# Performance work log

Hardware: AMD Instinct MI355X
Metric: run time of the kernel (lower is better)

The kernel has to match this reference:

```python
import jax, jax.numpy as jnp
import numpy as np

X = 512; Y = 512; C = 3; NK = 15
DT = 0.2; DD = 2; SIGMA = 0.95
THETA_X = 2.0; N_EXP = 2.0
K_SIZE = 16

# mesh-grid positions, cell centers at +0.5 (matches construct_mesh_grid)
POS = (jnp.stack(jnp.meshgrid(jnp.arange(X), jnp.arange(Y), indexing='ij'), axis=-1) + 0.5).astype(jnp.float32)  # [X,Y,2]


def _dwconv(img, k):
    # img [X,Y,C'] -> depthwise 3x3 cross-correlation with 'same' zero padding (matches torch conv2d)
    z = img.transpose(2, 0, 1)[None]                      # [1,C',X,Y]
    kern = jnp.tile(k[None, None], (z.shape[1], 1, 1, 1))  # [C',1,3,3]
    out = jax.lax.conv_general_dilated(z, kern, (1, 1), 'SAME', feature_group_count=z.shape[1])
    return out[0].transpose(1, 2, 0)


def _sobel(img):
    # returns [X,Y,2,C'] with (sy, sx) stacked on axis 2, matching torch code order
    kx = jnp.array([[-1., 0., 1.], [-2., 0., 2.], [-1., 0., 1.]], jnp.float32)
    return jnp.stack([_dwconv(img, kx.T), _dwconv(img, kx)], axis=2)


def _reintegrate(grid, F):
    # Flow-Lenia reintegration tracking: 25 static roll offsets, fused accumulation
    ma = DD - SIGMA
    mu = POS[..., None] + jnp.clip(DT * F, -ma, ma)  # [X,Y,2,C]
    mu = jnp.clip(mu, SIGMA, X - SIGMA)
    clip_hi = min(1.0, 2.0 * SIGMA)
    inv_area = 1.0 / (4.0 * SIGMA ** 2)
    acc = jnp.zeros_like(grid)
    for dx in range(-DD, DD + 1):
        for dy in range(-DD, DD + 1):
            gridR = jnp.roll(grid, (dx, dy), (0, 1))
            muR = jnp.roll(mu, (dx, dy), (0, 1))
            sz = 0.5 - jnp.abs(POS[..., None] - muR) + SIGMA
            area = jnp.prod(jnp.clip(sz, 0.0, clip_hi), axis=2) * inv_area  # [X,Y,C]
            acc = acc + gridR * area
    return acc


def _forward(x, Ks, m, s, h, w_c1, c0):
    # spectral kernels: normalize, fftshift, fft2 (matches construct_kernels)
    Ksn = Ks / Ks.sum(axis=(0, 1), keepdims=True)
    fk = jnp.fft.fft2(jnp.fft.fftshift(Ksn, axes=(0, 1)), axes=(0, 1))  # [X,Y,NK] complex
    fXs = jnp.fft.fft2(x, axes=(0, 1))
    Us = jnp.fft.ifft2(fk * fXs[:, :, c0], axes=(0, 1)).real            # [X,Y,NK]
    # growth * h (note: h appears again inside w_c1, faithful to original double multiply)
    Gs = (jnp.exp(-(((Us - m) / s) ** 2) * 0.5) * 2.0 - 1.0) * h
    Hs = jnp.einsum('xyk,kc->xyc', Gs, w_c1)                             # [X,Y,C]
    grad_u = _sobel(Hs)                                                  # [X,Y,2,C]
    grad_x = _sobel(x.sum(-1, keepdims=True))                            # [X,Y,2,1]
    alpha = jnp.clip((x[:, :, None, :] / THETA_X) ** N_EXP, 0.0, 1.0)    # [X,Y,1,C]
    F = grad_u * (1.0 - alpha) - grad_x * alpha                          # [X,Y,2,C]
    return _reintegrate(x, F)


def setup_inputs() -> dict:
    key = jax.random.key(0)
    k1, k2, k3, k4, k5 = jax.random.split(key, 5)
    x = jax.random.uniform(k1, (X, Y, C), jnp.float32)
    # ring kernels per construct_kernels (non-sparse branch)
    mg = np.mgrid[-X // 2:X // 2, -Y // 2:Y // 2]
    base = np.linalg.norm(mg, axis=0).astype(np.float32)
    ks_list = []
    for i in range(NK):
        r = 0.6 + 0.04 * i
        D = base / ((K_SIZE + 15) * r)
        sig = 0.5 * (np.tanh(-(D - 1.0) * 10.0 / 2.0) + 1.0)
        bell = np.exp(-(D - 0.5) ** 2 / 0.15)
        ks_list.append(sig * bell)
    Ks = jnp.asarray(np.stack(ks_list, -1).astype(np.float32))
    m = 0.1 + 0.3 * jax.random.uniform(k2, (NK,), jnp.float32)
    s = 0.03 + 0.15 * jax.random.uniform(k3, (NK,), jnp.float32)
    h = 0.3 + 0.7 * jax.random.uniform(k4, (NK,), jnp.float32)
    c0 = jax.random.randint(k5, (NK,), 0, C, jnp.int32)
    c1 = jnp.arange(NK) % C
    w_c1 = jax.nn.one_hot(c1, C, dtype=jnp.float32) * h[:, None]
    return {"x": x, "Ks": Ks, "m": m, "s": s, "h": h, "w_c1": w_c1, "c0": c0}


def reference(x, Ks, m, s, h, w_c1, c0):
    return _forward(x, Ks, m, s, h, w_c1, c0)
```

## Files before the change

### kernel.cpp

```cpp
#include <hip/hip_runtime.h>
#include <math.h>

#define NPIX 262144
#define NKER 15
#define PI_F 3.14159265358979323846f
#define HW 264
#define NCOL 264
#define CS 578
#define SK(n) ((n) + ((n) >> 3))

__device__ __forceinline__ float2 cadd(float2 a, float2 b) { return make_float2(a.x + b.x, a.y + b.y); }
__device__ __forceinline__ float2 csub(float2 a, float2 b) { return make_float2(a.x - b.x, a.y - b.y); }
__device__ __forceinline__ float2 cmul(float2 a, float2 b) {
  return make_float2(a.x * b.x - a.y * b.y, a.x * b.y + a.y * b.x);
}

__device__ __forceinline__ void fft_roots(int lane, float2* w1, float2* wh) {
  float s, c;
  sincosf(-2.0f * PI_F * (float)lane / 512.0f, &s, &c);
  *w1 = make_float2(c, s);
  int h = lane & ~7;
  *wh = make_float2(__shfl(c, h, 64), __shfl(s, h, 64));
}

template <bool INV>
__device__ __forceinline__ void dft8(float2 a[8]) {
  const float R = 0.70710678118654752f;
  float2 t0 = cadd(a[0], a[4]), u0 = csub(a[0], a[4]);
  float2 t1 = cadd(a[1], a[5]), u1 = csub(a[1], a[5]);
  float2 t2 = cadd(a[2], a[6]), u2 = csub(a[2], a[6]);
  float2 t3 = cadd(a[3], a[7]), u3 = csub(a[3], a[7]);
  u1 = INV ? make_float2(R * (u1.x - u1.y), R * (u1.x + u1.y))
           : make_float2(R * (u1.x + u1.y), R * (u1.y - u1.x));
  u2 = INV ? make_float2(-u2.y, u2.x) : make_float2(u2.y, -u2.x);
  u3 = INV ? make_float2(-R * (u3.x + u3.y), R * (u3.x - u3.y))
           : make_float2(R * (u3.y - u3.x), -R * (u3.x + u3.y));
  float2 e0 = cadd(t0, t2), f0 = csub(t0, t2);
  float2 e1 = cadd(t1, t3), f1 = csub(t1, t3);
  f1 = INV ? make_float2(-f1.y, f1.x) : make_float2(f1.y, -f1.x);
  float2 g0 = cadd(u0, u2), h0 = csub(u0, u2);
  float2 g1 = cadd(u1, u3), h1 = csub(u1, u3);
  h1 = INV ? make_float2(-h1.y, h1.x) : make_float2(h1.y, -h1.x);
  a[0] = cadd(e0, e1); a[4] = csub(e0, e1);
  a[2] = cadd(f0, f1); a[6] = csub(f0, f1);
  a[1] = cadd(g0, g1); a[5] = csub(g0, g1);
  a[3] = cadd(h0, h1); a[7] = csub(h0, h1);
}

template <bool INV>
__device__ __forceinline__ void fft512_r8(float2 a[8], float2* buf, int lane,
                                          float2 w1, float2 wh) {
  float2 wa = INV ? make_float2(w1.x, -w1.y) : w1;
  float2 wb = INV ? make_float2(wh.x, -wh.y) : wh;
  dft8<INV>(a);
  {
    float2 tq = wa;
    a[1] = cmul(a[1], tq);
#pragma unroll
    for (int q = 2; q < 8; ++q) { tq = cmul(tq, wa); a[q] = cmul(a[q], tq); }
  }
#pragma unroll
  for (int q = 0; q < 8; ++q) buf[9 * lane + q] = a[q];
#pragma unroll
  for (int q = 0; q < 8; ++q) a[q] = buf[SK(lane + 64 * q)];
  dft8<INV>(a);
  {
    float2 tq = wb;
    a[1] = cmul(a[1], tq);
#pragma unroll
    for (int q = 2; q < 8; ++q) { tq = cmul(tq, wb); a[q] = cmul(a[q], tq); }
  }
  int h = lane & ~7;
  int b2 = 9 * h + (lane - h);
#pragma unroll
  for (int q = 0; q < 8; ++q) buf[b2 + 9 * q] = a[q];
#pragma unroll
  for (int q = 0; q < 8; ++q) a[q] = buf[SK(lane + 64 * q)];
  dft8<INV>(a);
}

__device__ __forceinline__ void split_store_halfplane(float2 a[8], float2* buf, int lane,
                                                      float2* d0, float2* d1) {
#pragma unroll
  for (int q = 0; q < 8; ++q) buf[SK(lane + 64 * q)] = a[q];
#pragma unroll
  for (int q = 0; q < 4; ++q) {
    int v = lane + 64 * q;
    int mir = (512 - v) & 511;
    float2 P = a[q];
    float2 Qc = buf[SK(mir)];
    float2 Q = make_float2(Qc.x, -Qc.y);
    d0[v] = make_float2(0.5f * (P.x + Q.x), 0.5f * (P.y + Q.y));
    d1[v] = make_float2(0.5f * (P.y - Q.y), -0.5f * (P.x - Q.x));
  }
  if (lane == 0) {
    float2 P = a[4];
    d0[256] = make_float2(P.x, 0.f);
    d1[256] = make_float2(P.y, 0.f);
  }
}

__global__ void rows_all(const float* __restrict__ Ks, const float* __restrict__ x,
                         float* __restrict__ partial, float2* __restrict__ AkH,
                         float2* __restrict__ AxH) {
  __shared__ float krow[512 * NKER];
  __shared__ float2 scr[4][CS];
  __shared__ float psum[480];
  int t = threadIdx.x, wave = t >> 6, lane = t & 63;
  float2 w1, wh;
  fft_roots(lane, &w1, &wh);
  if (blockIdx.x < 512) {
    int b = blockIdx.x;
    int rs = (b + 256) & 511;
    const float2* src = (const float2*)Ks + (size_t)rs * 3840;
    float2* kr2 = (float2*)krow;
#pragma unroll
    for (int i = 0; i < 15; ++i) kr2[t + 256 * i] = src[t + 256 * i];
    __syncthreads();
    for (int i = t; i < 480; i += 256) {
      int k = i >> 5, yg = i & 31;
      float s = 0.f;
      int base = yg * 16;
#pragma unroll
      for (int y = 0; y < 16; ++y) s += krow[(base + y) * NKER + k];
      psum[i] = s;
    }
#pragma unroll
    for (int si = 0; si < 2; ++si) {
      int slot = wave + 4 * si;
      int k1 = 2 * slot, k2 = k1 + 1;
      float2 a[8];
#pragma unroll
      for (int q = 0; q < 8; ++q) {
        int ys = (lane + 64 * q + 256) & 511;
        float re = krow[ys * NKER + k1];
        float im = (k2 < NKER) ? krow[ys * NKER + k2] : 0.f;
        a[q] = make_float2(re, im);
      }
      fft512_r8<false>(a, &scr[wave][0], lane, w1, wh);
      float2* d0 = AkH + ((size_t)k1 * 512 + b) * HW;
      float2* d1 = AkH + ((size_t)k2 * 512 + b) * HW;
      split_store_halfplane(a, &scr[wave][0], lane, d0, d1);
    }
    __syncthreads();
    if (t < NKER) {
      float s = 0.f;
#pragma unroll
      for (int g = 0; g < 32; ++g) s += psum[(t << 5) + g];
      partial[b * 16 + t] = s;
    }
  } else {
    int b = blockIdx.x - 512;
    int c = b >> 6;
    int rp = (b & 63) * 4 + wave;
    int r0 = rp, r1 = rp + 256;
    float2 a[8];
#pragma unroll
    for (int q = 0; q < 8; ++q) {
      int y = lane + 64 * q;
      a[q] = make_float2(x[((size_t)r0 * 512 + y) * 3 + c],
                         x[((size_t)r1 * 512 + y) * 3 + c]);
    }
    fft512_r8<false>(a, &scr[wave][0], lane, w1, wh);
    float2* d0 = AxH + ((size_t)c * 512 + r0) * HW;
    float2* d1 = AxH + ((size_t)c * 512 + r1) * HW;
    split_store_halfplane(a, &scr[wave][0], lane, d0, d1);
  }
}

__global__ void mid_cols(const float2* __restrict__ AxH, float2* __restrict__ XHt,
                         const float* __restrict__ partial, float* __restrict__ sums) {
  __shared__ float2 buf[8 * CS];
  __shared__ float red[512];
  int t = threadIdx.x;
  if (blockIdx.x == 99) {
    int k = t & 15, g = t >> 4;
    float acc = 0.f;
    for (int b = g; b < 512; b += 32) acc += partial[b * 16 + k];
    red[t] = acc;
    __syncthreads();
    if (t < 16) {
      float s = 0.f;
#pragma unroll
      for (int g2 = 0; g2 < 32; ++g2) s += red[g2 * 16 + t];
      sums[t] = s;
    }
    return;
  }
  int ch = blockIdx.x / 33, slab = blockIdx.x % 33;
  int col0 = slab * 8;
  int c = t >> 6, lane = t & 63;
  float2 w1, wh;
  fft_roots(lane, &w1, &wh);
  const float2* bx = AxH + (size_t)ch * 512 * HW;
#pragma unroll
  for (int u = 0; u < 8; ++u) {
    int idx = (u << 9) + t;
    int row = idx >> 3, cc = idx & 7;
    buf[cc * CS + SK(row)] = bx[(size_t)row * HW + col0 + cc];
  }
  __syncthreads();
  float2 a[8];
#pragma unroll
  for (int q = 0; q < 8; ++q) a[q] = buf[c * CS + SK(lane + 64 * q)];
  fft512_r8<false>(a, &buf[c * CS], lane, w1, wh);
  float2* dst = XHt + ((size_t)ch * NCOL + col0 + c) * 512;
#pragma unroll
  for (int q = 0; q < 8; ++q) dst[lane + 64 * q] = a[q];
}

__global__ void fused_cols(float2* __restrict__ AkH, const float2* __restrict__ XHt,
                           const int* __restrict__ c0) {
  __shared__ float2 buf[8 * CS];
  int t = threadIdx.x, col0 = blockIdx.x * 8, k = blockIdx.y;
  int c = t >> 6, lane = t & 63;
  float2 w1, wh;
  fft_roots(lane, &w1, &wh);
  float2* bk = AkH + (size_t)k * 512 * HW;
  const float2* xcol = XHt + ((size_t)c0[k] * NCOL + col0 + c) * 512;
  float2 xh[8];
#pragma unroll
  for (int q = 0; q < 8; ++q) xh[q] = xcol[lane + 64 * q];
#pragma unroll
  for (int u = 0; u < 8; ++u) {
    int idx = (u << 9) + t;
    int row = idx >> 3, cc = idx & 7;
    buf[cc * CS + SK(row)] = bk[(size_t)row * HW + col0 + cc];
  }
  __syncthreads();
  float2 a[8];
#pragma unroll
  for (int q = 0; q < 8; ++q) a[q] = buf[c * CS + SK(lane + 64 * q)];
  fft512_r8<false>(a, &buf[c * CS], lane, w1, wh);
#pragma unroll
  for (int q = 0; q < 8; ++q) a[q] = cmul(a[q], xh[q]);
  fft512_r8<true>(a, &buf[c * CS], lane, w1, wh);
#pragma unroll
  for (int q = 0; q < 8; ++q) buf[c * CS + SK(lane + 64 * q)] = a[q];
  __syncthreads();
#pragma unroll
  for (int u = 0; u < 8; ++u) {
    int idx = (u << 9) + t;
    int row = idx >> 3, cc = idx & 7;
    bk[(size_t)row * HW + col0 + cc] = buf[cc * CS + SK(row)];
  }
}

__global__ void irows_growth_combine(const float2* __restrict__ AkH,
                                     const float* __restrict__ sums,
                                     const float* __restrict__ m, const float* __restrict__ s,
                                     const float* __restrict__ h, const float* __restrict__ w,
                                     float* __restrict__ Hs) {
  __shared__ float2 scr[4][CS];
  __shared__ float accL[4][3][512];
  __shared__ float mk[16], isk[16], hk[16], wk[16][3], sck[16];
  int t = threadIdx.x, wave = t >> 6, lane = t & 63;
  int row = blockIdx.x;
  if (t < NKER) {
    mk[t] = m[t]; isk[t] = 1.0f / s[t]; hk[t] = h[t];
    sck[t] = 1.0f / (sums[t] * 262144.0f);
    wk[t][0] = w[t * 3 + 0]; wk[t][1] = w[t * 3 + 1]; wk[t][2] = w[t * 3 + 2];
  }
  __syncthreads();
  float2 w1, wh;
  fft_roots(lane, &w1, &wh);
  float acc[3][8];
#pragma unroll
  for (int cc = 0; cc < 3; ++cc)
#pragma unroll
    for (int q = 0; q < 8; ++q) acc[cc][q] = 0.f;
  for (int si = 0; si < 2; ++si) {
    int slot = wave + 4 * si;
    int k1 = 2 * slot, k2 = 2 * slot + 1;
    bool dual = (k2 < NKER);
    const float2* p1 = AkH + ((size_t)k1 * 512 + row) * HW;
    const float2* p2 = AkH + ((size_t)(dual ? k2 : k1) * 512 + row) * HW;
    float2 a[8];
#pragma unroll
    for (int q = 0; q < 8; ++q) {
      int v = lane + 64 * q;
      if (v <= 256) {
        float2 A1 = p1[v];
        float2 A2 = dual ? p2[v] : make_float2(0.f, 0.f);
        a[q] = make_float2(A1.x - A2.y, A1.y + A2.x);
      } else {
        int mi = 512 - v;
        float2 A1 = p1[mi];
        float2 A2 = dual ? p2[mi] : make_float2(0.f, 0.f);
        a[q] = make_float2(A1.x + A2.y, -A1.y + A2.x);
      }
    }
    fft512_r8<true>(a, &scr[wave][0], lane, w1, wh);
    float m1 = mk[k1], i1 = isk[k1], h1 = hk[k1], s1 = sck[k1];
    float w10 = wk[k1][0], w11 = wk[k1][1], w12 = wk[k1][2];
#pragma unroll
    for (int q = 0; q < 8; ++q) {
      float tt = (a[q].x * s1 - m1) * i1;
      float g = (expf(-0.5f * tt * tt) * 2.0f - 1.0f) * h1;
      acc[0][q] += g * w10; acc[1][q] += g * w11; acc[2][q] += g * w12;
    }
    if (dual) {
      float m2 = mk[k2], i2 = isk[k2], h2 = hk[k2], s2 = sck[k2];
      float w20 = wk[k2][0], w21 = wk[k2][1], w22 = wk[k2][2];
#pragma unroll
      for (int q = 0; q < 8; ++q) {
        float tt = (a[q].y * s2 - m2) * i2;
        float g = (expf(-0.5f * tt * tt) * 2.0f - 1.0f) * h2;
        acc[0][q] += g * w20; acc[1][q] += g * w21; acc[2][q] += g * w22;
      }
    }
  }
#pragma unroll
  for (int cc = 0; cc < 3; ++cc)
#pragma unroll
    for (int q = 0; q < 8; ++q) accL[wave][cc][lane + 64 * q] = acc[cc][q];
  __syncthreads();
#pragma unroll
  for (int cc = 0; cc < 3; ++cc) {
#pragma unroll
    for (int rep = 0; rep < 2; ++rep) {
      int p = t + (rep << 8);
      float v = accL[0][cc][p] + accL[1][cc][p] + accL[2][cc][p] + accL[3][cc][p];
      Hs[(size_t)cc * NPIX + (size_t)row * 512 + p] = v;
    }
  }
}

__global__ void flow_reint(const float* __restrict__ x, const float* __restrict__ Hs,
                           float* __restrict__ out) {
  __shared__ float muT[20 * 20 * 6];
  __shared__ float xT[20 * 20 * 3];
  int ox = (blockIdx.x >> 5) << 4;
  int oy = (blockIdx.x & 31) << 4;
  for (int i = threadIdx.x; i < 400; i += 256) {
    int hi = i / 20, hj = i % 20;
    int qx = (ox - 2 + hi) & 511, qy = (oy - 2 + hj) & 511;
    float syH0 = 0.f, syH1 = 0.f, syH2 = 0.f;
    float sxH0 = 0.f, sxH1 = 0.f, sxH2 = 0.f;
    float syX = 0.f, sxX = 0.f;
#pragma unroll
    for (int di = -1; di <= 1; ++di) {
#pragma unroll
      for (int dj = -1; dj <= 1; ++dj) {
        if (di == 0 && dj == 0) continue;
        int xi = qx + di, yj = qy + dj;
        if ((unsigned)xi >= 512u || (unsigned)yj >= 512u) continue;
        float wy = (float)di * ((dj == 0) ? 2.f : 1.f);
        float wx = (float)dj * ((di == 0) ? 2.f : 1.f);
        int q = (xi << 9) | yj;
        float h0 = Hs[q], h1 = Hs[NPIX + q], h2 = Hs[2 * NPIX + q];
        syH0 += wy * h0; syH1 += wy * h1; syH2 += wy * h2;
        sxH0 += wx * h0; sxH1 += wx * h1; sxH2 += wx * h2;
        float xs = x[(size_t)q * 3 + 0] + x[(size_t)q * 3 + 1] + x[(size_t)q * 3 + 2];
        syX += wy * xs; sxX += wx * xs;
      }
    }
    int qp = (qx << 9) | qy;
    float cxq = (float)qx + 0.5f, cyq = (float)qy + 0.5f;
    float syH[3] = {syH0, syH1, syH2};
    float sxH[3] = {sxH0, sxH1, sxH2};
    int b6 = i * 6, b3 = i * 3;
#pragma unroll
    for (int c = 0; c < 3; ++c) {
      float xc = x[(size_t)qp * 3 + c];
      xT[b3 + c] = xc;
      float tt = xc * 0.5f;
      float alpha = fminf(tt * tt, 1.0f);
      float F0 = syH[c] * (1.f - alpha) - syX * alpha;
      float F1 = sxH[c] * (1.f - alpha) - sxX * alpha;
      float m0 = cxq + fminf(fmaxf(0.2f * F0, -1.05f), 1.05f);
      float m1 = cyq + fminf(fmaxf(0.2f * F1, -1.05f), 1.05f);
      muT[b6 + c]     = fminf(fmaxf(m0, 0.95f), 511.05f);
      muT[b6 + 3 + c] = fminf(fmaxf(m1, 0.95f), 511.05f);
    }
  }
  __syncthreads();
  int o = threadIdx.x;
  int lx = o >> 4, ly = o & 15;
  int px_ = ox + lx, py_ = oy + ly;
  float cx = (float)px_ + 0.5f, cy = (float)py_ + 0.5f;
  float a0 = 0.f, a1 = 0.f, a2 = 0.f;
#pragma unroll
  for (int dx = -2; dx <= 2; ++dx) {
    int hi = lx + 2 - dx;
#pragma unroll
    for (int dy = -2; dy <= 2; ++dy) {
      int hj = ly + 2 - dy;
      int b6 = (hi * 20 + hj) * 6, b3 = (hi * 20 + hj) * 3;
      float wv;
      wv = fminf(fmaxf(1.45f - fabsf(cx - muT[b6 + 0]), 0.f), 1.f) *
           fminf(fmaxf(1.45f - fabsf(cy - muT[b6 + 3]), 0.f), 1.f);
      a0 += xT[b3 + 0] * wv;
      wv = fminf(fmaxf(1.45f - fabsf(cx - muT[b6 + 1]), 0.f), 1.f) *
           fminf(fmaxf(1.45f - fabsf(cy - muT[b6 + 4]), 0.f), 1.f);
      a1 += xT[b3 + 1] * wv;
      wv = fminf(fmaxf(1.45f - fabsf(cx - muT[b6 + 2]), 0.f), 1.f) *
           fminf(fmaxf(1.45f - fabsf(cy - muT[b6 + 5]), 0.f), 1.f);
      a2 += xT[b3 + 2] * wv;
    }
  }
  const float inv_area = 0.27700831f;
  size_t p = (size_t)((px_ << 9) | py_);
  out[p * 3 + 0] = a0 * inv_area;
  out[p * 3 + 1] = a1 * inv_area;
  out[p * 3 + 2] = a2 * inv_area;
}

extern "C" void kernel_launch(void* const* d_in, const int* in_sizes, int n_in,
                              void* d_out, int out_size, void* d_ws, size_t ws_size,
                              hipStream_t stream) {
  const float* x    = (const float*)d_in[0];
  const float* Ks   = (const float*)d_in[1];
  const float* m    = (const float*)d_in[2];
  const float* s    = (const float*)d_in[3];
  const float* h    = (const float*)d_in[4];
  const float* w_c1 = (const float*)d_in[5];
  const int*   c0   = (const int*)d_in[6];
  float* out = (float*)d_out;

  char* ws = (char*)d_ws;
  size_t off = 0;
  float* sums    = (float*)(ws + off); off += 1024;
  float* partial = (float*)(ws + off); off += 512 * 16 * 4;
  float2* AxH  = (float2*)(ws + off); off += (size_t)3 * 512 * HW * 8;
  float2* XHt  = (float2*)(ws + off); off += (size_t)3 * NCOL * 512 * 8;
  float2* AkH  = (float2*)(ws + off); off += (size_t)16 * 512 * HW * 8;
  float*  Hs   = (float*)(ws + off);  off += (size_t)3 * NPIX * 4;

  rows_all<<<704, 256, 0, stream>>>(Ks, x, partial, AkH, AxH);
  mid_cols<<<100, 512, 0, stream>>>(AxH, XHt, partial, sums);
  fused_cols<<<dim3(33, NKER), 512, 0, stream>>>(AkH, XHt, c0);
  irows_growth_combine<<<512, 256, 0, stream>>>(AkH, sums, m, s, h, w_c1, Hs);
  flow_reint<<<1024, 256, 0, stream>>>(x, Hs, out);
}
```

Before: 135.4 us.

## Fuse x column FFT into per-kernel column pass and widen row blocks to 512 threads

Removes the separate mid_cols kernel and the XHt intermediate buffer. Each fused_cols block now redoes the column FFT of the matching x channel itself, and the kernel-sum reduction moves into an extra block column. rows_all and irows_growth_combine go to 512 threads so each wave handles one kernel pair instead of looping over two. This saves a launch and a global round trip, at the cost of 15x redundant x column FFTs and higher shared-memory and register use per block.

```diff
diff --git a/kernel.cpp b/kernel.cpp
--- a/kernel.cpp
+++ b/kernel.cpp
@@ -5,7 +5,6 @@
 #define NKER 15
 #define PI_F 3.14159265358979323846f
 #define HW 264
-#define NCOL 264
 #define CS 578
 #define SK(n) ((n) + ((n) >> 3))
 
@@ -104,7 +103,7 @@
                          float* __restrict__ partial, float2* __restrict__ AkH,
                          float2* __restrict__ AxH) {
   __shared__ float krow[512 * NKER];
-  __shared__ float2 scr[4][CS];
+  __shared__ float2 scr[8][CS];
   __shared__ float psum[480];
   int t = threadIdx.x, wave = t >> 6, lane = t & 63;
   float2 w1, wh;
@@ -114,21 +113,18 @@
     int rs = (b + 256) & 511;
     const float2* src = (const float2*)Ks + (size_t)rs * 3840;
     float2* kr2 = (float2*)krow;
-#pragma unroll
-    for (int i = 0; i < 15; ++i) kr2[t + 256 * i] = src[t + 256 * i];
+    for (int i = t; i < 3840; i += 512) kr2[i] = src[i];
     __syncthreads();
-    for (int i = t; i < 480; i += 256) {
-      int k = i >> 5, yg = i & 31;
+    if (t < 480) {
+      int k = t >> 5, yg = t & 31;
       float s = 0.f;
       int base = yg * 16;
 #pragma unroll
       for (int y = 0; y < 16; ++y) s += krow[(base + y) * NKER + k];
-      psum[i] = s;
-    }
-#pragma unroll
-    for (int si = 0; si < 2; ++si) {
-      int slot = wave + 4 * si;
-      int k1 = 2 * slot, k2 = k1 + 1;
+      psum[t] = s;
+    }
+    {
+      int k1 = 2 * wave, k2 = k1 + 1;
       float2 a[8];
 #pragma unroll
       for (int q = 0; q < 8; ++q) {
@@ -150,9 +146,9 @@
       partial[b * 16 + t] = s;
     }
   } else {
-    int b = blockIdx.x - 512;
-    int c = b >> 6;
-    int rp = (b & 63) * 4 + wave;
+    int job = (blockIdx.x - 512) * 8 + wave;
+    int c = job >> 8;
+    int rp = job & 255;
     int r0 = rp, r1 = rp + 256;
     float2 a[8];
 #pragma unroll
@@ -168,12 +164,14 @@
   }
 }
 
-__global__ void mid_cols(const float2* __restrict__ AxH, float2* __restrict__ XHt,
-                         const float* __restrict__ partial, float* __restrict__ sums) {
+__global__ void fused_cols(float2* __restrict__ AkH, const float2* __restrict__ AxH,
+                           const int* __restrict__ c0, const float* __restrict__ partial,
+                           float* __restrict__ sums) {
   __shared__ float2 buf[8 * CS];
   __shared__ float red[512];
   int t = threadIdx.x;
-  if (blockIdx.x == 99) {
+  if (blockIdx.x == 33) {
+    if (blockIdx.y != 0) return;
     int k = t & 15, g = t >> 4;
     float acc = 0.f;
     for (int b = g; b < 512; b += 32) acc += partial[b * 16 + k];
@@ -187,12 +185,12 @@
     }
     return;
   }
-  int ch = blockIdx.x / 33, slab = blockIdx.x % 33;
-  int col0 = slab * 8;
+  int col0 = blockIdx.x * 8, k = blockIdx.y;
   int c = t >> 6, lane = t & 63;
   float2 w1, wh;
   fft_roots(lane, &w1, &wh);
-  const float2* bx = AxH + (size_t)ch * 512 * HW;
+  const float2* bx = AxH + (size_t)c0[k] * 512 * HW;
+  float2* bk = AkH + (size_t)k * 512 * HW;
 #pragma unroll
   for (int u = 0; u < 8; ++u) {
     int idx = (u << 9) + t;
@@ -200,27 +198,11 @@
     buf[cc * CS + SK(row)] = bx[(size_t)row * HW + col0 + cc];
   }
   __syncthreads();
-  float2 a[8];
-#pragma unroll
-  for (int q = 0; q < 8; ++q) a[q] = buf[c * CS + SK(lane + 64 * q)];
-  fft512_r8<false>(a, &buf[c * CS], lane, w1, wh);
-  float2* dst = XHt + ((size_t)ch * NCOL + col0 + c) * 512;
-#pragma unroll
-  for (int q = 0; q < 8; ++q) dst[lane + 64 * q] = a[q];
-}
-
-__global__ void fused_cols(float2* __restrict__ AkH, const float2* __restrict__ XHt,
-                           const int* __restrict__ c0) {
-  __shared__ float2 buf[8 * CS];
-  int t = threadIdx.x, col0 = blockIdx.x * 8, k = blockIdx.y;
-  int c = t >> 6, lane = t & 63;
-  float2 w1, wh;
-  fft_roots(lane, &w1, &wh);
-  float2* bk = AkH + (size_t)k * 512 * HW;
-  const float2* xcol = XHt + ((size_t)c0[k] * NCOL + col0 + c) * 512;
   float2 xh[8];
 #pragma unroll
-  for (int q = 0; q < 8; ++q) xh[q] = xcol[lane + 64 * q];
+  for (int q = 0; q < 8; ++q) xh[q] = buf[c * CS + SK(lane + 64 * q)];
+  fft512_r8<false>(xh, &buf[c * CS], lane, w1, wh);
+  __syncthreads();
 #pragma unroll
   for (int u = 0; u < 8; ++u) {
     int idx = (u << 9) + t;
@@ -251,7 +233,7 @@
                                      const float* __restrict__ m, const float* __restrict__ s,
                                      const float* __restrict__ h, const float* __restrict__ w,
                                      float* __restrict__ Hs) {
-  __shared__ float2 scr[4][CS];
+  __shared__ float2 scr[8][CS];
   __shared__ float accL[4][3][512];
   __shared__ float mk[16], isk[16], hk[16], wk[16][3], sck[16];
   int t = threadIdx.x, wave = t >> 6, lane = t & 63;
@@ -269,8 +251,8 @@
   for (int cc = 0; cc < 3; ++cc)
 #pragma unroll
     for (int q = 0; q < 8; ++q) acc[cc][q] = 0.f;
-  for (int si = 0; si < 2; ++si) {
-    int slot = wave + 4 * si;
+  {
+    int slot = wave;
     int k1 = 2 * slot, k2 = 2 * slot + 1;
     bool dual = (k2 < NKER);
     const float2* p1 = AkH + ((size_t)k1 * 512 + row) * HW;
@@ -310,19 +292,24 @@
       }
     }
   }
-#pragma unroll
-  for (int cc = 0; cc < 3; ++cc)
-#pragma unroll
-    for (int q = 0; q < 8; ++q) accL[wave][cc][lane + 64 * q] = acc[cc][q];
+  if (wave < 4) {
+#pragma unroll
+    for (int cc = 0; cc < 3; ++cc)
+#pragma unroll
+      for (int q = 0; q < 8; ++q) accL[wave][cc][lane + 64 * q] = acc[cc][q];
+  }
+  __syncthreads();
+  if (wave >= 4) {
+#pragma unroll
+    for (int cc = 0; cc < 3; ++cc)
+#pragma unroll
+      for (int q = 0; q < 8; ++q) accL[wave - 4][cc][lane + 64 * q] += acc[cc][q];
+  }
   __syncthreads();
 #pragma unroll
   for (int cc = 0; cc < 3; ++cc) {
-#pragma unroll
-    for (int rep = 0; rep < 2; ++rep) {
-      int p = t + (rep << 8);
-      float v = accL[0][cc][p] + accL[1][cc][p] + accL[2][cc][p] + accL[3][cc][p];
-      Hs[(size_t)cc * NPIX + (size_t)row * 512 + p] = v;
-    }
+    float v = accL[0][cc][t] + accL[1][cc][t] + accL[2][cc][t] + accL[3][cc][t];
+    Hs[(size_t)cc * NPIX + (size_t)row * 512 + t] = v;
   }
 }
 
@@ -423,13 +410,11 @@
   float* sums    = (float*)(ws + off); off += 1024;
   float* partial = (float*)(ws + off); off += 512 * 16 * 4;
   float2* AxH  = (float2*)(ws + off); off += (size_t)3 * 512 * HW * 8;
-  float2* XHt  = (float2*)(ws + off); off += (size_t)3 * NCOL * 512 * 8;
   float2* AkH  = (float2*)(ws + off); off += (size_t)16 * 512 * HW * 8;
   float*  Hs   = (float*)(ws + off);  off += (size_t)3 * NPIX * 4;
 
-  rows_all<<<704, 256, 0, stream>>>(Ks, x, partial, AkH, AxH);
-  mid_cols<<<100, 512, 0, stream>>>(AxH, XHt, partial, sums);
-  fused_cols<<<dim3(33, NKER), 512, 0, stream>>>(AkH, XHt, c0);
-  irows_growth_combine<<<512, 256, 0, stream>>>(AkH, sums, m, s, h, w_c1, Hs);
+  rows_all<<<608, 512, 0, stream>>>(Ks, x, partial, AkH, AxH);
+  fused_cols<<<dim3(34, NKER), 512, 0, stream>>>(AkH, AxH, c0, partial, sums);
+  irows_growth_combine<<<512, 512, 0, stream>>>(AkH, sums, m, s, h, w_c1, Hs);
   flow_reint<<<1024, 256, 0, stream>>>(x, Hs, out);
 }
```

Result: no change. 133.2 us (median of 2 runs) (-1.7%).
